# Kernel tuning notes

Hardware: AMD Instinct MI355X
Metric: run time of the kernel (lower is better)

## Reference

```python
import jax, jax.numpy as jnp
import numpy as np

B = 64           # graphs
NPG = 2048       # nodes per graph
N = B * NPG      # total nodes
EPG = 32768      # edges per graph (avg degree 16)
E = B * EPG
D = 32           # in_features == out_features
RATIO = 0.5
K = int(NPG * RATIO)  # nodes kept per graph


def setup_inputs() -> dict:
    key = jax.random.key(0)
    ks = jax.random.split(key, 12)
    x = jax.random.normal(ks[0], (N, D), dtype=jnp.float32)
    gid = jnp.repeat(jnp.arange(B, dtype=jnp.int32), EPG)
    src = gid * NPG + jax.random.randint(ks[1], (E,), 0, NPG, dtype=jnp.int32)
    dst = gid * NPG + jax.random.randint(ks[2], (E,), 0, NPG, dtype=jnp.int32)
    edge_index = jnp.stack([src, dst])                      # [2, E]
    edge_attr = jax.random.uniform(ks[3], (E,), dtype=jnp.float32)
    batch = jnp.repeat(jnp.arange(B, dtype=jnp.int32), NPG)  # [N]
    s = 1.0 / np.sqrt(D)
    params = {}
    for i in range(3):
        params[f"W_root{i+1}"] = jax.random.normal(ks[4 + 2 * i], (D, D), dtype=jnp.float32) * s
        params[f"W_rel{i+1}"] = jax.random.normal(ks[5 + 2 * i], (D, D), dtype=jnp.float32) * s
        params[f"b{i+1}"] = jnp.zeros((D,), dtype=jnp.float32)
    return {"x": x, "edge_index": edge_index, "edge_attr": edge_attr, "batch": batch, **params}


def _graph_conv(x, src, dst, W_root, W_rel, b):
    # PyG GraphConv (aggr='add'): out_i = W_root x_i + W_rel * sum_{j->i} x_j + b
    agg = jax.ops.segment_sum(x[src], dst, num_segments=N)  # [N, D]
    return x @ W_root + agg @ W_rel + b


def reference(x, edge_index, edge_attr, batch,
              W_root1, W_rel1, b1, W_root2, W_rel2, b2, W_root3, W_rel3, b3):
    src, dst = edge_index[0], edge_index[1]
    x2 = _graph_conv(x, src, dst, W_root1, W_rel1, b1)  # [N, D]
    y2 = _graph_conv(x, src, dst, W_root2, W_rel2, b2)  # [N, D]
    # per-node attention score = <x2_i, y2_i> / sqrt(D)
    score = jnp.sum(x2 * y2, axis=-1) / jnp.sqrt(jnp.float32(D))  # [N]
    # topk per graph (equal-size graphs -> reshape + lax.top_k)
    _, top_idx = jax.lax.top_k(score.reshape(B, NPG), K)          # [B, K]
    perm = (top_idx + (jnp.arange(B, dtype=top_idx.dtype) * NPG)[:, None]).reshape(-1)  # [B*K]
    x3 = _graph_conv(x, src, dst, W_root3, W_rel3, b3)            # dropout_rate=0 -> identity
    # skip connection
    x5 = x[perm] + score[perm][:, None] * x3[perm]                # [B*K, D]
    new_batch = batch[perm]
    # filter_adj: relabel surviving nodes, mask (pad with -1 / 0) edges with a dropped endpoint
    new_idx = jnp.full((N,), -1, dtype=jnp.int32).at[perm].set(jnp.arange(perm.shape[0], dtype=jnp.int32))
    ns, nd = new_idx[src], new_idx[dst]
    valid = (ns >= 0) & (nd >= 0)
    new_edge_index = jnp.where(valid[None, :], jnp.stack([ns, nd]), -1)  # [2, E], -1 = dropped
    new_edge_attr = jnp.where(valid, edge_attr, 0.0)
    return (x5, new_edge_index, new_edge_attr, new_batch, perm, score[perm])
```

## Files before the change

kernel.cpp:

```cpp
#include <hip/hip_runtime.h>
#include <hip/hip_bf16.h>

#define NB   64
#define NPG  2048
#define NN   (NB*NPG)
#define EPG  32768
#define EE   (NB*EPG)
#define DD   32
#define KK   1024

#define QCAP 2560

typedef unsigned long long u64;
typedef unsigned int u32;

__global__ __launch_bounds__(1024) void qscatter_kernel(
    const int* __restrict__ src, const int* __restrict__ dst,
    int* __restrict__ qcnt, int* __restrict__ packed)
{
    __shared__ int wcnt[16][4];
    __shared__ int wbase[16][4];
    int b = blockIdx.x, t = threadIdx.x;
    int g = b & 63, s = b >> 6;
    int w = t >> 6, lane = t & 63;
    const int ebase = g * EPG + s * 8192;
    const int nbase = g * NPG;
    u64 ltmask = (1ull << lane) - 1ull;

    int pk[8], qv[8], pos[8];
    int wq0 = 0, wq1 = 0, wq2 = 0, wq3 = 0;
#pragma unroll
    for (int r = 0; r < 2; r++) {
        int e = ebase + r * 4096 + t * 4;
        int4 sv = *(const int4*)(src + e);
        int4 dv = *(const int4*)(dst + e);
        const int* sp = &sv.x; const int* dp = &dv.x;
#pragma unroll
        for (int m = 0; m < 4; m++) {
            int idx = r * 4 + m;
            int sl = sp[m] - nbase;
            int dl = dp[m] - nbase;
            int q  = dl >> 9;
            pk[idx] = (sl << 9) | (dl & 511);
            qv[idx] = q;
            u64 b0 = __ballot(q == 0);
            u64 b1 = __ballot(q == 1);
            u64 b2 = __ballot(q == 2);
            u64 b3 = __ballot(q == 3);
            int rk = (q == 0) ? wq0 + __popcll(b0 & ltmask)
                   : (q == 1) ? wq1 + __popcll(b1 & ltmask)
                   : (q == 2) ? wq2 + __popcll(b2 & ltmask)
                              : wq3 + __popcll(b3 & ltmask);
            pos[idx] = rk;
            wq0 += __popcll(b0); wq1 += __popcll(b1);
            wq2 += __popcll(b2); wq3 += __popcll(b3);
        }
    }
    if (lane == 0) {
        wcnt[w][0] = wq0; wcnt[w][1] = wq1;
        wcnt[w][2] = wq2; wcnt[w][3] = wq3;
    }
    __syncthreads();
    if (t < 4) {
        int run = 0;
        for (int ww = 0; ww < 16; ww++) { wbase[ww][t] = run; run += wcnt[ww][t]; }
        qcnt[((s * 64 + g) << 2) + t] = run;
    }
    __syncthreads();
    const int rbase = (s * 64 + g) << 2;
#pragma unroll
    for (int r = 0; r < 8; r++) {
        int q = qv[r];
        packed[(size_t)(rbase + q) * QCAP + wbase[w][q] + pos[r]] = pk[r];
    }
}

__global__ __launch_bounds__(1024) void agg2_kernel(
    const float* __restrict__ x,
    const int* __restrict__ qcnt, const int* __restrict__ packed,
    float* __restrict__ agg)
{
    __shared__ int acc[512 * DD];
    int b = blockIdx.x, t = threadIdx.x;
    int g = b & 63, q = b >> 6;
    for (int i = t; i < 512 * DD; i += 1024) acc[i] = 0;
    __syncthreads();

    const float SCALE = 4194304.0f;
    const float* xg = x + (size_t)g * NPG * DD;
    int sub   = t & 3;
    int ei0   = t >> 2;
    int dbase = sub << 3;

    for (int s = 0; s < 4; s++) {
        int n = qcnt[((s * 64 + g) << 2) + q];
        const int* pb = packed + (size_t)(((s * 64 + g) << 2) + q) * QCAP;
        for (int i = ei0; i < n; i += 256) {
            int pkv = pb[i];
            int dl  = pkv & 511;
            int sl  = pkv >> 9;
            const float4* xp = (const float4*)(xg + sl * DD + dbase);
            float4 v0 = xp[0];
            float4 v1 = xp[1];
            int* ar = acc + (dl << 5);
            int  m  = dl & 31;
            atomicAdd(ar + ((dbase + 0) ^ m), __float2int_rn(v0.x * SCALE));
            atomicAdd(ar + ((dbase + 1) ^ m), __float2int_rn(v0.y * SCALE));
            atomicAdd(ar + ((dbase + 2) ^ m), __float2int_rn(v0.z * SCALE));
            atomicAdd(ar + ((dbase + 3) ^ m), __float2int_rn(v0.w * SCALE));
            atomicAdd(ar + ((dbase + 4) ^ m), __float2int_rn(v1.x * SCALE));
            atomicAdd(ar + ((dbase + 5) ^ m), __float2int_rn(v1.y * SCALE));
            atomicAdd(ar + ((dbase + 6) ^ m), __float2int_rn(v1.z * SCALE));
            atomicAdd(ar + ((dbase + 7) ^ m), __float2int_rn(v1.w * SCALE));
        }
    }
    __syncthreads();

    const float ISCALE = 2.38418579101562e-07f;
    float* ao = agg + ((size_t)g * NPG + (size_t)q * 512) * DD;
    for (int i = t; i < 512 * DD; i += 1024) {
        int row = i >> 5, d = i & 31;
        ao[i] = (float)acc[(row << 5) | (d ^ (row & 31))] * ISCALE;
    }
}

__global__ __launch_bounds__(256) void score_kernel(
    const float* __restrict__ x, const float* __restrict__ agg,
    const float* __restrict__ Wr1, const float* __restrict__ Wl1, const float* __restrict__ b1,
    const float* __restrict__ Wr2, const float* __restrict__ Wl2, const float* __restrict__ b2,
    float* __restrict__ score)
{
    __shared__ float4 sWr1[DD*DD/4], sWl1[DD*DD/4], sWr2[DD*DD/4], sWl2[DD*DD/4];
    __shared__ float sb1[DD], sb2[DD];
    __shared__ float2 part[128];
    {
        int t = threadIdx.x;
        sWr1[t] = ((const float4*)Wr1)[t];
        sWl1[t] = ((const float4*)Wl1)[t];
        sWr2[t] = ((const float4*)Wr2)[t];
        sWl2[t] = ((const float4*)Wl2)[t];
        if (t < DD) { sb1[t] = b1[t]; sb2[t] = b2[t]; }
    }
    __syncthreads();

    int lane = threadIdx.x & 127;
    int half = threadIdx.x >> 7;
    int i0 = blockIdx.x * 128 + lane;
    int i1 = i0 + NN/2;

    float xv0[DD], av0[DD], xv1[DD], av1[DD];
    {
        const float4* xp0 = (const float4*)(x + (long long)i0 * DD);
        const float4* ap0 = (const float4*)(agg + (long long)i0 * DD);
        const float4* xp1 = (const float4*)(x + (long long)i1 * DD);
        const float4* ap1 = (const float4*)(agg + (long long)i1 * DD);
#pragma unroll
        for (int q = 0; q < 8; q++) {
            float4 v0 = xp0[q]; xv0[4*q]=v0.x; xv0[4*q+1]=v0.y; xv0[4*q+2]=v0.z; xv0[4*q+3]=v0.w;
            float4 w0 = ap0[q]; av0[4*q]=w0.x; av0[4*q+1]=w0.y; av0[4*q+2]=w0.z; av0[4*q+3]=w0.w;
            float4 v1 = xp1[q]; xv1[4*q]=v1.x; xv1[4*q+1]=v1.y; xv1[4*q+2]=v1.z; xv1[4*q+3]=v1.w;
            float4 w1 = ap1[q]; av1[4*q]=w1.x; av1[4*q+1]=w1.y; av1[4*q+2]=w1.z; av1[4*q+3]=w1.w;
        }
    }

    float sc0 = 0.f, sc1 = 0.f;
    int dbase = half * 4;
    for (int dd = 0; dd < 4; dd++) {
        int d0 = dbase + dd;
        float a0[4], q0[4], a1[4], q1[4];
#pragma unroll
        for (int j = 0; j < 4; j++) {
            a0[j] = sb1[4*d0+j]; q0[j] = sb2[4*d0+j];
            a1[j] = sb1[4*d0+j]; q1[j] = sb2[4*d0+j];
        }
#pragma unroll
        for (int k = 0; k < DD; k++) {
            float4 wr1 = sWr1[k*8 + d0];
            float4 wl1 = sWl1[k*8 + d0];
            float4 wr2 = sWr2[k*8 + d0];
            float4 wl2 = sWl2[k*8 + d0];
            const float* r1 = &wr1.x; const float* l1 = &wl1.x;
            const float* r2 = &wr2.x; const float* l2 = &wl2.x;
            float xk0 = xv0[k], ak0 = av0[k];
            float xk1 = xv1[k], ak1 = av1[k];
#pragma unroll
            for (int j = 0; j < 4; j++) {
                a0[j] += xk0 * r1[j];
                a0[j] += ak0 * l1[j];
                q0[j] += xk0 * r2[j];
                q0[j] += ak0 * l2[j];
                a1[j] += xk1 * r1[j];
                a1[j] += ak1 * l1[j];
                q1[j] += xk1 * r2[j];
                q1[j] += ak1 * l2[j];
            }
        }
#pragma unroll
        for (int j = 0; j < 4; j++) { sc0 += a0[j] * q0[j]; sc1 += a1[j] * q1[j]; }
    }

    if (half) { part[lane].x = sc0; part[lane].y = sc1; }
    __syncthreads();
    if (!half) {
        float2 p = part[lane];
        score[i0] = (sc0 + p.x) * 0.17677669529663687f;
        score[i1] = (sc1 + p.y) * 0.17677669529663687f;
    }
}

__device__ __forceinline__ u64 shfl_xor_u64(u64 v, int j) {
    u32 lo = (u32)v, hi = (u32)(v >> 32);
    lo = (u32)__shfl_xor((int)lo, j, 64);
    hi = (u32)__shfl_xor((int)hi, j, 64);
    return ((u64)hi << 32) | lo;
}

__device__ __forceinline__ void reg_step(u64& v, int e, int j, int k) {
    u64 vp = shfl_xor_u64(v, j);
    bool upper   = (e & j) != 0;
    bool asc     = (e & k) == 0;
    bool takemax = (upper == asc);
    bool gt      = v > vp;
    v = (gt == takemax) ? v : vp;
}

__global__ __launch_bounds__(1024) void topk_kernel(
    const float* __restrict__ score,
    int* __restrict__ perm_int, int* __restrict__ new_idx,
    float* __restrict__ out_perm,
    float* __restrict__ out_batch,
    float* __restrict__ out_score)
{
    __shared__ u64 keys[NPG];
    int b = blockIdx.x;
    int t = threadIdx.x;
    const float* s = score + (long long)b * NPG;
    int w = t >> 6, ln = t & 63;
    int e0 = w * 128 + ln, e1 = e0 + 64;

    u64 k0, k1;
    {
        u32 u = __float_as_uint(s[e0]);
        u32 h = (u & 0x80000000u) ? u : ~(u | 0x80000000u);
        k0 = ((u64)h << 32) | (u32)e0;
        u = __float_as_uint(s[e1]);
        h = (u & 0x80000000u) ? u : ~(u | 0x80000000u);
        k1 = ((u64)h << 32) | (u32)e1;
    }

    for (int k = 2; k <= 128; k <<= 1) {
        for (int j = k >> 1; j >= 1; j >>= 1) {
            if (j == 64) {
                bool asc = (e0 & k) == 0;
                u64 mx = (k0 > k1) ? k0 : k1;
                u64 mn = (k0 > k1) ? k1 : k0;
                k0 = asc ? mn : mx;
                k1 = asc ? mx : mn;
            } else {
                reg_step(k0, e0, j, k);
                reg_step(k1, e1, j, k);
            }
        }
    }

    for (int k = 256; k <= NPG; k <<= 1) {
        keys[e0] = k0; keys[e1] = k1;
        __syncthreads();
        for (int j = k >> 1; j >= 128; j >>= 1) {
            int i = ((t & ~(j - 1)) << 1) | (t & (j - 1));
            int l = i | j;
            u64 a = keys[i], c = keys[l];
            bool up = ((i & k) == 0);
            if ((a > c) == up) { keys[i] = c; keys[l] = a; }
            __syncthreads();
        }
        k0 = keys[e0]; k1 = keys[e1];
        for (int j = 64; j >= 1; j >>= 1) {
            if (j == 64) {
                bool asc = (e0 & k) == 0;
                u64 mx = (k0 > k1) ? k0 : k1;
                u64 mn = (k0 > k1) ? k1 : k0;
                k0 = asc ? mn : mx;
                k1 = asc ? mx : mn;
            } else {
                reg_step(k0, e0, j, k);
                reg_step(k1, e1, j, k);
            }
        }
    }

    keys[e0] = k0; keys[e1] = k1;
    __syncthreads();

    u64 kk = keys[t];
    int idx = (int)(u32)(kk & 0xFFFFFFFFu);
    int g = b * NPG + idx;
    int o = b * KK + t;
    perm_int[o] = g;
    new_idx[g] = o;
    out_perm[o]  = (float)g;
    out_batch[o] = (float)b;
    out_score[o] = s[idx];

    u64 kd = keys[t + KK];
    int idxd = (int)(u32)(kd & 0xFFFFFFFFu);
    new_idx[b * NPG + idxd] = -1;
}

__global__ __launch_bounds__(256) void x5_kernel(
    const float* __restrict__ x, const float* __restrict__ agg,
    const float* __restrict__ Wr3, const float* __restrict__ Wl3, const float* __restrict__ b3,
    const int* __restrict__ perm_int, const float* __restrict__ score,
    float* __restrict__ out_x5)
{
    __shared__ float4 sWr[DD*DD/4], sWl[DD*DD/4];
    __shared__ float sb[DD];
    {
        int t = threadIdx.x;
        sWr[t] = ((const float4*)Wr3)[t];
        sWl[t] = ((const float4*)Wl3)[t];
        if (t < DD) sb[t] = b3[t];
    }
    __syncthreads();

    int lane = threadIdx.x & 127;
    int half = threadIdx.x >> 7;
    int i = blockIdx.x * 128 + lane;
    int g = perm_int[i];
    float sc = score[g];

    float xv[DD], av[DD];
    {
        const float4* xp = (const float4*)(x + (long long)g * DD);
        const float4* ap = (const float4*)(agg + (long long)g * DD);
#pragma unroll
        for (int q = 0; q < 8; q++) {
            float4 v = xp[q]; xv[4*q]=v.x; xv[4*q+1]=v.y; xv[4*q+2]=v.z; xv[4*q+3]=v.w;
            float4 w = ap[q]; av[4*q]=w.x; av[4*q+1]=w.y; av[4*q+2]=w.z; av[4*q+3]=w.w;
        }
    }

    float* outp = out_x5 + (long long)i * DD;
    int dbase = half * 4;
    for (int dd = 0; dd < 4; dd++) {
        int d0 = dbase + dd;
        float a[4];
#pragma unroll
        for (int j = 0; j < 4; j++) a[j] = sb[4*d0+j];
#pragma unroll
        for (int k = 0; k < DD; k++) {
            float xk = xv[k], ak = av[k];
            float4 wr = sWr[k*8 + d0];
            float4 wl = sWl[k*8 + d0];
            const float* rp = &wr.x; const float* lp = &wl.x;
#pragma unroll
            for (int j = 0; j < 4; j++) {
                a[j] += xk * rp[j];
                a[j] += ak * lp[j];
            }
        }
#pragma unroll
        for (int j = 0; j < 4; j++) outp[4*d0+j] = xv[4*d0+j] + sc * a[j];
    }
}

__global__ __launch_bounds__(256) void edge_kernel(
    const int* __restrict__ src, const int* __restrict__ dst,
    const float* __restrict__ edge_attr,
    const int* __restrict__ new_idx,
    float* __restrict__ out_ei,
    float* __restrict__ out_attr)
{
    int e = (blockIdx.x * 256 + threadIdx.x) * 4;
    if (e >= EE) return;
    int4 s4 = *(const int4*)(src + e);
    int4 d4 = *(const int4*)(dst + e);
    float4 at = *(const float4*)(edge_attr + e);

    int ns[4] = { new_idx[s4.x], new_idx[s4.y], new_idx[s4.z], new_idx[s4.w] };
    int nd[4] = { new_idx[d4.x], new_idx[d4.y], new_idx[d4.z], new_idx[d4.w] };
    float av[4] = { at.x, at.y, at.z, at.w };

    float4 os, od, oa;
    float* osp = &os.x; float* odp = &od.x; float* oap = &oa.x;
#pragma unroll
    for (int j = 0; j < 4; j++) {
        bool valid = (ns[j] >= 0) && (nd[j] >= 0);
        osp[j] = (float)(valid ? ns[j] : -1);
        odp[j] = (float)(valid ? nd[j] : -1);
        oap[j] = valid ? av[j] : 0.f;
    }
    *(float4*)(out_ei + e)      = os;
    *(float4*)(out_ei + EE + e) = od;
    *(float4*)(out_attr + e)    = oa;
}

extern "C" void kernel_launch(void* const* d_in, const int* in_sizes, int n_in,
                              void* d_out, int out_size, void* d_ws, size_t ws_size,
                              hipStream_t stream)
{
    const float* x     = (const float*)d_in[0];
    const int*   src   = (const int*)d_in[1];
    const int*   dst   = ((const int*)d_in[1]) + EE;
    const float* eattr = (const float*)d_in[2];
    const float* Wr1 = (const float*)d_in[4];
    const float* Wl1 = (const float*)d_in[5];
    const float* b1  = (const float*)d_in[6];
    const float* Wr2 = (const float*)d_in[7];
    const float* Wl2 = (const float*)d_in[8];
    const float* b2  = (const float*)d_in[9];
    const float* Wr3 = (const float*)d_in[10];
    const float* Wl3 = (const float*)d_in[11];
    const float* b3  = (const float*)d_in[12];

    char* ws = (char*)d_ws;
    float* score    = (float*)(ws + 0);
    int*   perm_int = (int*)  (ws + (size_t)NN*4);
    int*   new_idx  = (int*)  (ws + (size_t)NN*4 + (size_t)NB*KK*4);
    int*   qcnt     = (int*)  (ws + (size_t)NN*8 + (size_t)NB*KK*4);
    int*   packed   = (int*)  (ws + (size_t)NN*8 + (size_t)NB*KK*4 + 4096);

    float* out = (float*)d_out;
    float* out_x5    = out;
    float* out_ei    = out + (size_t)NB*KK*DD;
    float* out_attr  = out_ei + (size_t)2*EE;
    float* out_batch = out_attr + (size_t)EE;
    float* out_perm  = out_batch + (size_t)NB*KK;
    float* out_score = out_perm + (size_t)NB*KK;

    float* agg = out_ei;

    qscatter_kernel<<<256, 1024, 0, stream>>>(src, dst, qcnt, packed);

    agg2_kernel<<<256, 1024, 0, stream>>>(x, qcnt, packed, agg);

    score_kernel<<<NN/256, 256, 0, stream>>>(x, agg, Wr1, Wl1, b1, Wr2, Wl2, b2, score);

    topk_kernel<<<NB, 1024, 0, stream>>>(score, perm_int, new_idx,
                                         out_perm, out_batch, out_score);

    x5_kernel<<<(NB*KK)/128, 256, 0, stream>>>(x, agg, Wr3, Wl3, b3,
                                               perm_int, score, out_x5);

    edge_kernel<<<(EE/4)/256, 256, 0, stream>>>(src, dst, eattr, new_idx, out_ei, out_attr);
}
```

Measured before the change: 206.0 us.

## Compute one node per thread in score kernel with weights read from global

The score kernel now assigns one node per thread and computes all 32 output features directly. Weights and biases are read from global memory with uniform addresses, where they can be served by scalar loads and constant cache, instead of being staged in shared memory. This removes the LDS staging, the barrier and the cross-half partial-sum exchange. In exchange it raises register pressure (64 accumulators plus 64 inputs per thread), which could cut occupancy or cause spills.

```diff
diff --git a/kernel.cpp b/kernel.cpp
--- a/kernel.cpp
+++ b/kernel.cpp
@@ -130,82 +130,45 @@
     const float* __restrict__ Wr2, const float* __restrict__ Wl2, const float* __restrict__ b2,
     float* __restrict__ score)
 {
-    __shared__ float4 sWr1[DD*DD/4], sWl1[DD*DD/4], sWr2[DD*DD/4], sWl2[DD*DD/4];
-    __shared__ float sb1[DD], sb2[DD];
-    __shared__ float2 part[128];
+    int i = blockIdx.x * 256 + threadIdx.x;
+
+    float xv[DD], av[DD];
     {
-        int t = threadIdx.x;
-        sWr1[t] = ((const float4*)Wr1)[t];
-        sWl1[t] = ((const float4*)Wl1)[t];
-        sWr2[t] = ((const float4*)Wr2)[t];
-        sWl2[t] = ((const float4*)Wl2)[t];
-        if (t < DD) { sb1[t] = b1[t]; sb2[t] = b2[t]; }
-    }
-    __syncthreads();
-
-    int lane = threadIdx.x & 127;
-    int half = threadIdx.x >> 7;
-    int i0 = blockIdx.x * 128 + lane;
-    int i1 = i0 + NN/2;
-
-    float xv0[DD], av0[DD], xv1[DD], av1[DD];
-    {
-        const float4* xp0 = (const float4*)(x + (long long)i0 * DD);
-        const float4* ap0 = (const float4*)(agg + (long long)i0 * DD);
-        const float4* xp1 = (const float4*)(x + (long long)i1 * DD);
-        const float4* ap1 = (const float4*)(agg + (long long)i1 * DD);
+        const float4* xp = (const float4*)(x + (long long)i * DD);
+        const float4* ap = (const float4*)(agg + (long long)i * DD);
 #pragma unroll
         for (int q = 0; q < 8; q++) {
-            float4 v0 = xp0[q]; xv0[4*q]=v0.x; xv0[4*q+1]=v0.y; xv0[4*q+2]=v0.z; xv0[4*q+3]=v0.w;
-            float4 w0 = ap0[q]; av0[4*q]=w0.x; av0[4*q+1]=w0.y; av0[4*q+2]=w0.z; av0[4*q+3]=w0.w;
-            float4 v1 = xp1[q]; xv1[4*q]=v1.x; xv1[4*q+1]=v1.y; xv1[4*q+2]=v1.z; xv1[4*q+3]=v1.w;
-            float4 w1 = ap1[q]; av1[4*q]=w1.x; av1[4*q+1]=w1.y; av1[4*q+2]=w1.z; av1[4*q+3]=w1.w;
-        }
-    }
-
-    float sc0 = 0.f, sc1 = 0.f;
-    int dbase = half * 4;
-    for (int dd = 0; dd < 4; dd++) {
-        int d0 = dbase + dd;
-        float a0[4], q0[4], a1[4], q1[4];
-#pragma unroll
-        for (int j = 0; j < 4; j++) {
-            a0[j] = sb1[4*d0+j]; q0[j] = sb2[4*d0+j];
-            a1[j] = sb1[4*d0+j]; q1[j] = sb2[4*d0+j];
-        }
-#pragma unroll
-        for (int k = 0; k < DD; k++) {
-            float4 wr1 = sWr1[k*8 + d0];
-            float4 wl1 = sWl1[k*8 + d0];
-            float4 wr2 = sWr2[k*8 + d0];
-            float4 wl2 = sWl2[k*8 + d0];
-            const float* r1 = &wr1.x; const float* l1 = &wl1.x;
-            const float* r2 = &wr2.x; const float* l2 = &wl2.x;
-            float xk0 = xv0[k], ak0 = av0[k];
-            float xk1 = xv1[k], ak1 = av1[k];
-#pragma unroll
-            for (int j = 0; j < 4; j++) {
-                a0[j] += xk0 * r1[j];
-                a0[j] += ak0 * l1[j];
-                q0[j] += xk0 * r2[j];
-                q0[j] += ak0 * l2[j];
-                a1[j] += xk1 * r1[j];
-                a1[j] += ak1 * l1[j];
-                q1[j] += xk1 * r2[j];
-                q1[j] += ak1 * l2[j];
-            }
-        }
-#pragma unroll
-        for (int j = 0; j < 4; j++) { sc0 += a0[j] * q0[j]; sc1 += a1[j] * q1[j]; }
-    }
-
-    if (half) { part[lane].x = sc0; part[lane].y = sc1; }
-    __syncthreads();
-    if (!half) {
-        float2 p = part[lane];
-        score[i0] = (sc0 + p.x) * 0.17677669529663687f;
-        score[i1] = (sc1 + p.y) * 0.17677669529663687f;
-    }
+            float4 v = xp[q]; xv[4*q]=v.x; xv[4*q+1]=v.y; xv[4*q+2]=v.z; xv[4*q+3]=v.w;
+            float4 w = ap[q]; av[4*q]=w.x; av[4*q+1]=w.y; av[4*q+2]=w.z; av[4*q+3]=w.w;
+        }
+    }
+
+    float a[DD], qy[DD];
+#pragma unroll
+    for (int d = 0; d < DD; d++) { a[d] = b1[d]; qy[d] = b2[d]; }
+
+#pragma unroll
+    for (int k = 0; k < DD; k++) {
+        float xk = xv[k], ak = av[k];
+        const float* r1 = Wr1 + k * DD;
+        const float* l1 = Wl1 + k * DD;
+        const float* r2 = Wr2 + k * DD;
+        const float* l2 = Wl2 + k * DD;
+#pragma unroll
+        for (int d = 0; d < DD; d++) {
+            a[d]  += xk * r1[d];
+            a[d]  += ak * l1[d];
+            qy[d] += xk * r2[d];
+            qy[d] += ak * l2[d];
+        }
+    }
+
+    float s0 = 0.f, s1 = 0.f;
+#pragma unroll
+    for (int d = 0; d < 16; d++) s0 += a[d] * qy[d];
+#pragma unroll
+    for (int d = 16; d < DD; d++) s1 += a[d] * qy[d];
+    score[i] = (s0 + s1) * 0.17677669529663687f;
 }
 
 __device__ __forceinline__ u64 shfl_xor_u64(u64 v, int j) {
```

Measured after the change: 294.1 us. 42.8% more time.
